# Kernel optimization log

Hardware: AMD Instinct MI355X
Metric: run time of the kernel (lower is better)

## Reference

```python
import jax, jax.numpy as jnp
import numpy as np

N, E, B = 24000, 96000, 1200
NPG = N // B  # nodes per graph

def _lin(k, fi, fo):
    s = 1.0 / np.sqrt(fi)
    return jax.random.uniform(k, (fi, fo), jnp.float32, -s, s)

def setup_inputs():
    key = jax.random.key(0)
    ks = jax.random.split(key, 32)
    x = jax.random.normal(ks[0], (N, 9), jnp.float32)
    edge_attr = jax.random.normal(ks[1], (E, 4), jnp.float32)
    src = jax.random.randint(ks[2], (E,), 0, N)
    # destination node within the same graph as the source (block-diagonal adjacency)
    dst = (src // NPG) * NPG + jax.random.randint(ks[3], (E,), 0, NPG)
    edge_index = jnp.stack([src, dst]).astype(jnp.int32)
    batch = (jnp.arange(N) // NPG).astype(jnp.int32)
    fp_batch = jax.random.normal(ks[4], (B, 2048), jnp.float32)
    p = dict(
        Wq1=_lin(ks[5], 9, 512), bq1=jnp.zeros(512, jnp.float32),
        Wk1=_lin(ks[6], 9, 512), bk1=jnp.zeros(512, jnp.float32),
        Wv1=_lin(ks[7], 9, 512), bv1=jnp.zeros(512, jnp.float32),
        We1=_lin(ks[8], 4, 512),
        Ws1=_lin(ks[9], 9, 512), bs1=jnp.zeros(512, jnp.float32),
        Wq2=_lin(ks[10], 512, 1024), bq2=jnp.zeros(1024, jnp.float32),
        Wk2=_lin(ks[11], 512, 1024), bk2=jnp.zeros(1024, jnp.float32),
        Wv2=_lin(ks[12], 512, 1024), bv2=jnp.zeros(1024, jnp.float32),
        We2=_lin(ks[13], 4, 1024),
        Ws2=_lin(ks[14], 512, 1024), bs2=jnp.zeros(1024, jnp.float32),
        Wfp=_lin(ks[15], 2048, 256), bfp=jnp.zeros(256, jnp.float32),
        Wfin=_lin(ks[16], 1280, 1024), bfin=jnp.zeros(1024, jnp.float32),
    )
    return dict(x=x, edge_index=edge_index, edge_attr=edge_attr, batch=batch, fp_batch=fp_batch, **p)

def _tconv(x, src, dst, ea, Wq, bq, Wk, bk, Wv, bv, We, Ws, bs, H, C):
    """PyG TransformerConv: concat=True, beta=False, root_weight=True."""
    n = x.shape[0]
    q = (x @ Wq + bq).reshape(n, H, C)
    k = (x @ Wk + bk).reshape(n, H, C)
    v = (x @ Wv + bv).reshape(n, H, C)
    e = (ea @ We).reshape(-1, H, C)            # lin_edge has no bias
    ke = k[src] + e                            # [E,H,C]
    alpha = jnp.einsum('ehc,ehc->eh', q[dst], ke) / jnp.sqrt(jnp.float32(C))
    # scatter-softmax over incoming edges of each target node
    amax = jax.ops.segment_max(alpha, dst, num_segments=n)
    amax = jnp.where(jnp.isfinite(amax), amax, 0.0)  # nodes with no in-edges
    ex = jnp.exp(alpha - amax[dst])
    den = jax.ops.segment_sum(ex, dst, num_segments=n)[dst] + 1e-16
    msg = (v[src] + e) * (ex / den)[:, :, None]
    out = jax.ops.segment_sum(msg, dst, num_segments=n).reshape(n, H * C)
    return out + x @ Ws + bs                   # root/skip connection

def reference(x, edge_index, edge_attr, batch, fp_batch, Wq1, bq1, Wk1, bk1, Wv1, bv1, We1, Ws1, bs1, Wq2, bq2, Wk2, bk2, Wv2, bv2, We2, Ws2, bs2, Wfp, bfp, Wfin, bfin):
    src, dst = edge_index[0], edge_index[1]
    h = jax.nn.relu(_tconv(x, src, dst, edge_attr, Wq1, bq1, Wk1, bk1, Wv1, bv1, We1, Ws1, bs1, 4, 128))
    h = _tconv(h, src, dst, edge_attr, Wq2, bq2, Wk2, bk2, Wv2, bv2, We2, Ws2, bs2, 4, 256)
    cnt = jax.ops.segment_sum(jnp.ones((h.shape[0],), h.dtype), batch, num_segments=B)
    g = jax.ops.segment_sum(h, batch, num_segments=B) / cnt[:, None]  # global_mean_pool
    fp = fp_batch @ Wfp + bfp
    return jnp.concatenate([g, fp], axis=-1) @ Wfin + bfin
```

## Files before the change

kernel.cpp:

```cpp
#include <hip/hip_runtime.h>
#include <cstdint>
#include <cstddef>

static constexpr int NN = 24000;
static constexpr int NE = 96000;
static constexpr int NB = 1200;
static constexpr int NPG = 20;
static constexpr int MPAD = 24064;

typedef __attribute__((ext_vector_type(8))) short bfv8;
typedef __attribute__((ext_vector_type(4))) float fv4;

__device__ __forceinline__ unsigned f2ord(float f){
  unsigned u = __float_as_uint(f);
  return (u & 0x80000000u) ? ~u : (u | 0x80000000u);
}
__device__ __forceinline__ float ord2f(unsigned u){
  return (u & 0x80000000u) ? __uint_as_float(u & 0x7FFFFFFFu)
                           : __uint_as_float(~u);
}
__device__ __forceinline__ unsigned short f2bf(float f){
  unsigned u = __float_as_uint(f);
  u += 0x7FFFu + ((u >> 16) & 1u);
  return (unsigned short)(u >> 16);
}
__device__ __forceinline__ float bf2f(unsigned short s){
  return __uint_as_float(((unsigned)s) << 16);
}

__global__ __launch_bounds__(256) void count_kernel(const int* __restrict__ dst,
                                                    unsigned* __restrict__ deg)
{
  int e = blockIdx.x*256 + threadIdx.x;
  if (e < NE) atomicAdd(&deg[dst[e]], 1u);
}

__global__ __launch_bounds__(1024) void scan_kernel(const unsigned* __restrict__ deg,
                                                    unsigned* __restrict__ rowstart)
{
  __shared__ unsigned s[1024];
  __shared__ unsigned carry_s;
  int tid = threadIdx.x;
  if (tid == 0) carry_s = 0;
  __syncthreads();
  for (int base = 0; base < NN; base += 1024){
    unsigned v = (base + tid < NN) ? deg[base + tid] : 0u;
    s[tid] = v;
    __syncthreads();
#pragma unroll
    for (int off = 1; off < 1024; off <<= 1){
      unsigned t = (tid >= off) ? s[tid - off] : 0u;
      __syncthreads();
      s[tid] += t;
      __syncthreads();
    }
    unsigned carry = carry_s;
    if (base + tid < NN) rowstart[base + tid] = carry + s[tid] - v;
    __syncthreads();
    if (tid == 0) carry_s = carry + s[1023];
    __syncthreads();
  }
  if (tid == 0) rowstart[NN] = carry_s;
}

__global__ __launch_bounds__(256) void scatter_kernel(const int* __restrict__ dst,
                                                      const unsigned* __restrict__ rowstart,
                                                      unsigned* __restrict__ cur,
                                                      int* __restrict__ eidx)
{
  int e = blockIdx.x*256 + threadIdx.x;
  if (e >= NE) return;
  int d = dst[e];
  unsigned p = rowstart[d] + atomicAdd(&cur[d], 1u);
  eidx[p] = e;
}

__global__ __launch_bounds__(256) void node_gemm_l1_pair(
    const float* __restrict__ x,
    const float* __restrict__ Wa, const float* __restrict__ ba,
    const float* __restrict__ Wb, const float* __restrict__ bb,
    float* __restrict__ outa, float* __restrict__ outb)
{
  int t = blockIdx.x*256 + threadIdx.x;
  if (t >= NN*512) return;
  int n = t >> 9, j = t & 511;
  float xr[9];
#pragma unroll
  for (int i=0;i<9;i++) xr[i] = x[n*9+i];
  float aa=ba[j], ab=bb[j];
#pragma unroll
  for (int i=0;i<9;i++){
    float xi = xr[i];
    aa += xi*Wa[i*512+j];
    ab += xi*Wb[i*512+j];
  }
  outa[t]=aa; outb[t]=ab;
}

__global__ __launch_bounds__(256) void alpha_f32_kernel(
    const float* __restrict__ q, const float* __restrict__ k,
    const float* __restrict__ ea, const float* __restrict__ We,
    const int* __restrict__ src, const int* __restrict__ dst,
    float* __restrict__ alpha, unsigned* __restrict__ amax)
{
  constexpr int C = 128, HC = 512;
  int wave = (blockIdx.x*256 + threadIdx.x) >> 6;
  int lane = threadIdx.x & 63;
  if (wave >= NE) return;
  int e = wave;
  int s = src[e], d = dst[e];
  float ea0=ea[e*4+0], ea1=ea[e*4+1], ea2=ea[e*4+2], ea3=ea[e*4+3];
  const float scale = 1.0f / sqrtf((float)C);
#pragma unroll
  for (int h=0;h<4;h++){
    float part = 0.f;
#pragma unroll
    for (int c0=0;c0<C;c0+=64){
      int f = h*C + c0 + lane;
      float ke = k[(size_t)s*HC + f]
               + ea0*We[0*HC+f] + ea1*We[1*HC+f] + ea2*We[2*HC+f] + ea3*We[3*HC+f];
      part += q[(size_t)d*HC + f] * ke;
    }
#pragma unroll
    for (int off=32; off>=1; off>>=1) part += __shfl_xor(part, off);
    if (lane==0){
      float a = part*scale;
      alpha[e*4+h] = a;
      atomicMax(&amax[d*4+h], f2ord(a));
    }
  }
}

__global__ __launch_bounds__(256) void alpha_bf16_kernel(
    const unsigned short* __restrict__ q, const unsigned short* __restrict__ k,
    const float* __restrict__ ea, const float* __restrict__ We,
    const int* __restrict__ src, const int* __restrict__ dst,
    float* __restrict__ alpha, unsigned* __restrict__ amax)
{
  int wave = (blockIdx.x*256 + threadIdx.x) >> 6;
  int lane = threadIdx.x & 63;
  if (wave >= NE) return;
  int e = wave;
  int s = src[e], d = dst[e];
  float ea0=ea[e*4+0], ea1=ea[e*4+1], ea2=ea[e*4+2], ea3=ea[e*4+3];
  const float scale = 1.0f/16.0f;
#pragma unroll
  for (int p=0;p<2;p++){
    int off = p*512 + lane*8;
    bfv8 qv = *reinterpret_cast<const bfv8*>(q + (size_t)d*1024 + off);
    bfv8 kv = *reinterpret_cast<const bfv8*>(k + (size_t)s*1024 + off);
    float part = 0.f;
#pragma unroll
    for (int j=0;j<8;j++){
      int f = off + j;
      float ef = ea0*We[f] + ea1*We[1024+f] + ea2*We[2048+f] + ea3*We[3072+f];
      part += bf2f((unsigned short)qv[j]) * (bf2f((unsigned short)kv[j]) + ef);
    }
#pragma unroll
    for (int o=16; o>=1; o>>=1) part += __shfl_xor(part, o);
    if ((lane & 31) == 0){
      int h = p*2 + (lane>>5);
      float a = part*scale;
      alpha[e*4+h] = a;
      atomicMax(&amax[d*4+h], f2ord(a));
    }
  }
}

__global__ __launch_bounds__(256) void ex_kernel(
    float* __restrict__ alpha, const unsigned* __restrict__ amax,
    const int* __restrict__ dst, float* __restrict__ den)
{
  int t = blockIdx.x*256 + threadIdx.x;
  if (t >= NE*4) return;
  int e = t>>2, h = t&3;
  int d = dst[e];
  float m = ord2f(amax[d*4+h]);
  float v = __expf(alpha[t]-m);
  alpha[t] = v;
  unsafeAtomicAdd(&den[d*4+h], v);
}

__global__ __launch_bounds__(256) void gather512_kernel(
    const float* __restrict__ v, const float* __restrict__ ea,
    const float* __restrict__ We,
    const int* __restrict__ src,
    const unsigned* __restrict__ rowstart, const int* __restrict__ eidx,
    const float* __restrict__ exw, const float* __restrict__ den,
    float* __restrict__ acc)
{
  int n = blockIdx.x;
  int tid = threadIdx.x;
  int h = tid >> 6;
  int f2 = tid*2;
  unsigned p0 = rowstart[n], p1 = rowstart[n+1];
  float2 W0 = *reinterpret_cast<const float2*>(We + 0*512 + f2);
  float2 W1 = *reinterpret_cast<const float2*>(We + 1*512 + f2);
  float2 W2 = *reinterpret_cast<const float2*>(We + 2*512 + f2);
  float2 W3 = *reinterpret_cast<const float2*>(We + 3*512 + f2);
  float rdn = 1.0f / (den[n*4+h] + 1e-16f);
  float2 s = *reinterpret_cast<float2*>(acc + (size_t)n*512 + f2);
  for (unsigned p = p0; p < p1; ++p){
    int e  = eidx[p];
    float w = exw[e*4+h] * rdn;
    float4 eav = *reinterpret_cast<const float4*>(ea + (size_t)e*4);
    float2 vv  = *reinterpret_cast<const float2*>(v + (size_t)src[e]*512 + f2);
    float efx = eav.x*W0.x + eav.y*W1.x + eav.z*W2.x + eav.w*W3.x;
    float efy = eav.x*W0.y + eav.y*W1.y + eav.z*W2.y + eav.w*W3.y;
    s.x += w*(vv.x + efx);
    s.y += w*(vv.y + efy);
  }
  *reinterpret_cast<float2*>(acc + (size_t)n*512 + f2) = s;
}

__global__ __launch_bounds__(256) void gather1024_kernel(
    const float* __restrict__ v, const float* __restrict__ ea,
    const float* __restrict__ We,
    const int* __restrict__ src,
    const unsigned* __restrict__ rowstart, const int* __restrict__ eidx,
    const float* __restrict__ exw, const float* __restrict__ den,
    float* __restrict__ acc)
{
  int n = blockIdx.x;
  int tid = threadIdx.x;
  int h = tid >> 6;
  int f4 = tid*4;
  unsigned p0 = rowstart[n], p1 = rowstart[n+1];
  float4 W0 = *reinterpret_cast<const float4*>(We + 0*1024 + f4);
  float4 W1 = *reinterpret_cast<const float4*>(We + 1*1024 + f4);
  float4 W2 = *reinterpret_cast<const float4*>(We + 2*1024 + f4);
  float4 W3 = *reinterpret_cast<const float4*>(We + 3*1024 + f4);
  float rdn = 1.0f / (den[n*4+h] + 1e-16f);
  float4 s = *reinterpret_cast<float4*>(acc + (size_t)n*1024 + f4);
  for (unsigned p = p0; p < p1; ++p){
    int e  = eidx[p];
    float w = exw[e*4+h] * rdn;
    float4 eav = *reinterpret_cast<const float4*>(ea + (size_t)e*4);
    float4 vv  = *reinterpret_cast<const float4*>(v + (size_t)src[e]*1024 + f4);
    s.x += w*(vv.x + eav.x*W0.x + eav.y*W1.x + eav.z*W2.x + eav.w*W3.x);
    s.y += w*(vv.y + eav.x*W0.y + eav.y*W1.y + eav.z*W2.y + eav.w*W3.y);
    s.z += w*(vv.z + eav.x*W0.z + eav.y*W1.z + eav.z*W2.z + eav.w*W3.z);
    s.w += w*(vv.w + eav.x*W0.w + eav.y*W1.w + eav.z*W2.w + eav.w*W3.w);
  }
  *reinterpret_cast<float4*>(acc + (size_t)n*1024 + f4) = s;
}

__global__ __launch_bounds__(256) void relu_kernel(float* __restrict__ a, size_t n)
{
  size_t t = (size_t)blockIdx.x*256 + threadIdx.x;
  if (t < n) a[t] = fmaxf(a[t], 0.0f);
}

__global__ __launch_bounds__(256) void cvt_bf16_kernel(const float* __restrict__ in,
                                                       unsigned short* __restrict__ out,
                                                       size_t n)
{
  size_t t = (size_t)blockIdx.x*256 + threadIdx.x;
  if (t < n) out[t] = f2bf(in[t]);
}

__global__ __launch_bounds__(256) void cvt_wt_kernel(const float* __restrict__ W,
                                                     unsigned short* __restrict__ Wt)
{
  int t = blockIdx.x*256 + threadIdx.x;
  if (t >= 1024*512) return;
  int n = t >> 9, k = t & 511;
  Wt[t] = f2bf(W[k*1024 + n]);
}

template<bool BOUT>
__global__ __launch_bounds__(256) void gemm_bf16_mfma(
    const unsigned short* __restrict__ A,
    const unsigned short* __restrict__ B,
    const float* __restrict__ bias,
    void* __restrict__ Cout, int M)
{
  constexpr int K = 512, N = 1024;
  __shared__ unsigned short As[128*32];
  __shared__ unsigned short Bs[128*32];
  int tid  = threadIdx.x;
  int wid  = tid >> 6, lane = tid & 63;
  int wr   = wid >> 1, wc = wid & 1;
  int bm   = blockIdx.y * 128, bn = blockIdx.x * 128;
  int l15  = lane & 15, kg = lane >> 4;

  int r0 = (wid*2+0)*16 + (lane>>2);
  int r1 = (wid*2+1)*16 + (lane>>2);
  int s0 = lane & 3;
  int kc0 = s0 ^ ((r0>>1)&3);
  int kc1 = s0 ^ ((r1>>1)&3);
  unsigned short* ldsA0 = As + (wid*2+0)*512;
  unsigned short* ldsA1 = As + (wid*2+1)*512;
  unsigned short* ldsB0 = Bs + (wid*2+0)*512;
  unsigned short* ldsB1 = Bs + (wid*2+1)*512;

  fv4 acc[4][4];
#pragma unroll
  for (int m=0;m<4;m++)
#pragma unroll
    for (int n=0;n<4;n++) acc[m][n] = (fv4){0.f,0.f,0.f,0.f};

  for (int k0 = 0; k0 < K; k0 += 32){
    __syncthreads();
    __builtin_amdgcn_global_load_lds(
        (const __attribute__((address_space(1))) void*)(A + (size_t)(bm+r0)*K + k0 + kc0*8),
        (__attribute__((address_space(3))) void*)ldsA0, 16, 0, 0);
    __builtin_amdgcn_global_load_lds(
        (const __attribute__((address_space(1))) void*)(A + (size_t)(bm+r1)*K + k0 + kc1*8),
        (__attribute__((address_space(3))) void*)ldsA1, 16, 0, 0);
    __builtin_amdgcn_global_load_lds(
        (const __attribute__((address_space(1))) void*)(B + (size_t)(bn+r0)*K + k0 + kc0*8),
        (__attribute__((address_space(3))) void*)ldsB0, 16, 0, 0);
    __builtin_amdgcn_global_load_lds(
        (const __attribute__((address_space(1))) void*)(B + (size_t)(bn+r1)*K + k0 + kc1*8),
        (__attribute__((address_space(3))) void*)ldsB1, 16, 0, 0);
    __syncthreads();
    bfv8 af[4], bfr[4];
#pragma unroll
    for (int m=0;m<4;m++){
      int r  = wr*64 + m*16 + l15;
      int sl = kg ^ ((r>>1)&3);
      af[m] = *reinterpret_cast<const bfv8*>(reinterpret_cast<char*>(As) + r*64 + sl*16);
    }
#pragma unroll
    for (int n=0;n<4;n++){
      int r  = wc*64 + n*16 + l15;
      int sl = kg ^ ((r>>1)&3);
      bfr[n] = *reinterpret_cast<const bfv8*>(reinterpret_cast<char*>(Bs) + r*64 + sl*16);
    }
#pragma unroll
    for (int m=0;m<4;m++)
#pragma unroll
      for (int n=0;n<4;n++)
        acc[m][n] = __builtin_amdgcn_mfma_f32_16x16x32_bf16(af[m], bfr[n], acc[m][n], 0, 0, 0);
  }
#pragma unroll
  for (int m=0;m<4;m++){
#pragma unroll
    for (int n=0;n<4;n++){
      int col = bn + wc*64 + n*16 + l15;
      float bcol = bias[col];
#pragma unroll
      for (int r=0;r<4;r++){
        int row = bm + wr*64 + m*16 + (lane>>4)*4 + r;
        if (row < M){
          float val = acc[m][n][r] + bcol;
          if (BOUT) ((unsigned short*)Cout)[(size_t)row*N + col] = f2bf(val);
          else      ((float*)Cout)[(size_t)row*N + col] = val;
        }
      }
    }
  }
}

__global__ __launch_bounds__(256) void sgemm_partial(
    const float* __restrict__ A, const float* __restrict__ W,
    float* __restrict__ P, int M, int N, int K, int kchunk, int zoff)
{
  __shared__ float As[32][68];
  __shared__ __align__(16) float Bs[32][64];
  int tid = threadIdx.x;
  int bm = blockIdx.y*64, bn = blockIdx.x*64;
  int kbeg = blockIdx.z*kchunk;
  int kend = min(kbeg + kchunk, K);
  float* Pz = P + (size_t)(zoff + blockIdx.z)*M*N;
  int ty = tid >> 4, tx = tid & 15;
  float acc[4][4] = {};
  for (int k0 = kbeg; k0 < kend; k0 += 32){
#pragma unroll
    for (int i=0;i<2;i++){
      int lin = tid + i*256;
      int r = lin >> 3;
      int kq = (lin & 7) * 4;
      float4 av = make_float4(0.f,0.f,0.f,0.f);
      int row = bm + r;
      if (row < M) av = *reinterpret_cast<const float4*>(A + (size_t)row*K + k0 + kq);
      As[kq+0][r]=av.x; As[kq+1][r]=av.y; As[kq+2][r]=av.z; As[kq+3][r]=av.w;
    }
#pragma unroll
    for (int i=0;i<2;i++){
      int lin = tid + i*256;
      int kr = lin >> 4;
      int c4 = (lin & 15) * 4;
      float4 wv = *reinterpret_cast<const float4*>(W + (size_t)(k0+kr)*N + bn + c4);
      *reinterpret_cast<float4*>(&Bs[kr][c4]) = wv;
    }
    __syncthreads();
#pragma unroll
    for (int kk=0;kk<32;kk++){
      float a[4], b[4];
#pragma unroll
      for (int i=0;i<4;i++) a[i] = As[kk][ty*4+i];
#pragma unroll
      for (int j=0;j<4;j++) b[j] = Bs[kk][tx*4+j];
#pragma unroll
      for (int i=0;i<4;i++)
#pragma unroll
        for (int j=0;j<4;j++) acc[i][j] += a[i]*b[j];
    }
    __syncthreads();
  }
#pragma unroll
  for (int i=0;i<4;i++){
    int row = bm + ty*4 + i;
    if (row >= M) break;
#pragma unroll
    for (int j=0;j<4;j++)
      Pz[(size_t)row*N + bn + tx*4 + j] = acc[i][j];
  }
}

__global__ __launch_bounds__(256) void reduce_add_kernel(
    const float* __restrict__ P, const float* __restrict__ bias,
    float* __restrict__ O, int total, int nz, int nmask)
{
  int t = blockIdx.x*256 + threadIdx.x;
  if (t >= total) return;
  float s = bias[t & nmask];
  for (int z = 0; z < nz; ++z) s += P[(size_t)z*total + t];
  O[t] = s;
}

__global__ __launch_bounds__(256) void pool_kernel(const float* __restrict__ h2,
                                                   float* __restrict__ g)
{
  int t = blockIdx.x*256 + threadIdx.x;
  if (t >= NB*256) return;
  int b = t >> 8, f4 = (t & 255) * 4;
  float4 s = make_float4(0.f,0.f,0.f,0.f);
#pragma unroll
  for (int i=0;i<NPG;i++){
    float4 v = *reinterpret_cast<const float4*>(h2 + (size_t)(b*NPG+i)*1024 + f4);
    s.x += v.x; s.y += v.y; s.z += v.z; s.w += v.w;
  }
  s.x *= (1.0f/NPG); s.y *= (1.0f/NPG); s.z *= (1.0f/NPG); s.w *= (1.0f/NPG);
  *reinterpret_cast<float4*>(g + (size_t)b*1024 + f4) = s;
}

extern "C" void kernel_launch(void* const* d_in, const int* in_sizes, int n_in,
                              void* d_out, int out_size, void* d_ws, size_t ws_size,
                              hipStream_t stream)
{
  const float* x    = (const float*)d_in[0];
  const int*   ei   = (const int*)d_in[1];
  const float* ea   = (const float*)d_in[2];
  const float* fpb  = (const float*)d_in[4];
  const float* Wq1  = (const float*)d_in[5];  const float* bq1 = (const float*)d_in[6];
  const float* Wk1  = (const float*)d_in[7];  const float* bk1 = (const float*)d_in[8];
  const float* Wv1  = (const float*)d_in[9];  const float* bv1 = (const float*)d_in[10];
  const float* We1  = (const float*)d_in[11];
  const float* Ws1  = (const float*)d_in[12]; const float* bs1 = (const float*)d_in[13];
  const float* Wq2  = (const float*)d_in[14]; const float* bq2 = (const float*)d_in[15];
  const float* Wk2  = (const float*)d_in[16]; const float* bk2 = (const float*)d_in[17];
  const float* Wv2  = (const float*)d_in[18]; const float* bv2 = (const float*)d_in[19];
  const float* We2  = (const float*)d_in[20];
  const float* Ws2  = (const float*)d_in[21]; const float* bs2 = (const float*)d_in[22];
  const float* Wfp  = (const float*)d_in[23]; const float* bfp = (const float*)d_in[24];
  const float* Wfin = (const float*)d_in[25]; const float* bfin= (const float*)d_in[26];
  const int* src = ei;
  const int* dst = ei + NE;
  float* out = (float*)d_out;

  const size_t F512  = (size_t)NN*512;
  const size_t F1024 = (size_t)NN*1024;
  float* base = (float*)d_ws;
  float* C_a = base;
  float* C_b = base + F1024;
  float* H   = base + 2*F1024;
  float* qv1 = C_a;
  unsigned short* q2b = (unsigned short*)C_a;
  unsigned short* k2b = (unsigned short*)C_b;
  unsigned short* hb  = (unsigned short*)H;
  unsigned short* WtQ = hb + (size_t)MPAD*512;
  unsigned short* WtK = WtQ + (size_t)1024*512;
  unsigned short* WtV = WtK + (size_t)1024*512;
  unsigned short* WtS = WtV + (size_t)1024*512;
  unsigned short* hbT = (unsigned short*)C_a;
  float* P1 = C_a;
  float* P2 = C_a + 5*(size_t)NB*1024;

  float* tail = base + 2*F1024 + F512;
  float*    alphab   = tail;
  unsigned* amax     = (unsigned*)(alphab + (size_t)NE*4);
  float*    den      = (float*)(amax + (size_t)NN*4);
  unsigned* deg      = (unsigned*)(den + (size_t)NN*4);
  unsigned* cur      = deg + NN;
  unsigned* rowstart = cur + NN;
  int*      eidx     = (int*)(rowstart + NN + 1);
  float*    g        = (float*)(eidx + NE);
  float*    fp       = g + (size_t)NB*1024;

  hipMemsetAsync(deg, 0, sizeof(unsigned)*NN, stream);
  hipMemsetAsync(cur, 0, sizeof(unsigned)*NN, stream);
  count_kernel<<<(NE+255)/256, 256, 0, stream>>>(dst, deg);
  scan_kernel<<<1, 1024, 0, stream>>>(deg, rowstart);
  scatter_kernel<<<(NE+255)/256, 256, 0, stream>>>(dst, rowstart, cur, eidx);

  hipMemsetAsync(amax, 0, sizeof(unsigned)*(size_t)NN*4, stream);
  hipMemsetAsync(den,  0, sizeof(float)*(size_t)NN*4, stream);

  node_gemm_l1_pair<<<(NN*512+255)/256, 256, 0, stream>>>(x, Wq1,bq1, Wk1,bk1, qv1, H);
  alpha_f32_kernel<<<NE/4, 256, 0, stream>>>(qv1, H, ea, We1, src, dst, alphab, amax);
  ex_kernel<<<(NE*4+255)/256, 256, 0, stream>>>(alphab, amax, dst, den);
  node_gemm_l1_pair<<<(NN*512+255)/256, 256, 0, stream>>>(x, Wv1,bv1, Ws1,bs1, qv1, H);
  gather512_kernel<<<NN, 256, 0, stream>>>(qv1, ea, We1, src, rowstart, eidx, alphab, den, H);
  relu_kernel<<<(int)((F512+255)/256), 256, 0, stream>>>(H, F512);

  cvt_bf16_kernel<<<(int)((F512+255)/256), 256, 0, stream>>>(H, hbT, F512);
  hipMemcpyAsync(hb, hbT, F512*sizeof(unsigned short), hipMemcpyDeviceToDevice, stream);
  hipMemsetAsync(hb + F512, 0, (size_t)(MPAD-NN)*512*sizeof(unsigned short), stream);
  cvt_wt_kernel<<<(1024*512+255)/256, 256, 0, stream>>>(Wq2, WtQ);
  cvt_wt_kernel<<<(1024*512+255)/256, 256, 0, stream>>>(Wk2, WtK);
  cvt_wt_kernel<<<(1024*512+255)/256, 256, 0, stream>>>(Wv2, WtV);
  cvt_wt_kernel<<<(1024*512+255)/256, 256, 0, stream>>>(Ws2, WtS);

  hipMemsetAsync(amax, 0, sizeof(unsigned)*(size_t)NN*4, stream);
  hipMemsetAsync(den,  0, sizeof(float)*(size_t)NN*4, stream);

  {
    dim3 grid(8, MPAD/128);
    gemm_bf16_mfma<true><<<grid, 256, 0, stream>>>(hb, WtQ, bq2, q2b, NN);
    gemm_bf16_mfma<true><<<grid, 256, 0, stream>>>(hb, WtK, bk2, k2b, NN);
  }
  alpha_bf16_kernel<<<NE/4, 256, 0, stream>>>(q2b, k2b, ea, We2, src, dst, alphab, amax);
  ex_kernel<<<(NE*4+255)/256, 256, 0, stream>>>(alphab, amax, dst, den);
  {
    dim3 grid(8, MPAD/128);
    gemm_bf16_mfma<false><<<grid, 256, 0, stream>>>(hb, WtV, bv2, C_a, NN);
    gemm_bf16_mfma<false><<<grid, 256, 0, stream>>>(hb, WtS, bs2, C_b, NN);
  }
  gather1024_kernel<<<NN, 256, 0, stream>>>(C_a, ea, We2, src, rowstart, eidx, alphab, den, C_b);

  pool_kernel<<<(NB*256+255)/256, 256, 0, stream>>>(C_b, g);

  {
    dim3 gfp(256/64, (NB+63)/64, 8);
    sgemm_partial<<<gfp, 256, 0, stream>>>(fpb, Wfp, P2, NB, 256, 2048, 256, 0);
    reduce_add_kernel<<<(NB*256+255)/256, 256, 0, stream>>>(P2, bfp, fp, NB*256, 8, 255);
  }
  {
    dim3 g1(1024/64, (NB+63)/64, 4);
    sgemm_partial<<<g1, 256, 0, stream>>>(g, Wfin, P1, NB, 1024, 1024, 256, 0);
    dim3 g2(1024/64, (NB+63)/64, 1);
    sgemm_partial<<<g2, 256, 0, stream>>>(fp, Wfin + (size_t)1024*1024, P1, NB, 1024, 256, 256, 4);
    reduce_add_kernel<<<(NB*1024+255)/256, 256, 0, stream>>>(P1, bfin, out, NB*1024, 5, 1023);
  }
}
```

Baseline: 922.7 us.

## Store layer-1 Q/K/V and layer-2 V in bf16, fuse relu+convert into gather

Layer-1 node projections for Q, K and V are written as bf16, and the layer-1 alpha kernel reads bf16 vectors with a 16-lane head reduction. The layer-1 gather now applies relu and writes bf16 output directly into the GEMM input buffer. This removes the separate relu, convert and memcpy kernels. The layer-2 V GEMM also emits bf16, so the gather reads half the bytes. The cost is lower precision in the attention logits and messages, plus reworked buffer aliasing.

```diff
diff --git a/kernel.cpp b/kernel.cpp
--- a/kernel.cpp
+++ b/kernel.cpp
@@ -75,11 +75,12 @@
   eidx[p] = e;
 }
 
+template<bool BA, bool BB>
 __global__ __launch_bounds__(256) void node_gemm_l1_pair(
     const float* __restrict__ x,
     const float* __restrict__ Wa, const float* __restrict__ ba,
     const float* __restrict__ Wb, const float* __restrict__ bb,
-    float* __restrict__ outa, float* __restrict__ outb)
+    void* __restrict__ outa, void* __restrict__ outb)
 {
   int t = blockIdx.x*256 + threadIdx.x;
   if (t >= NN*512) return;
@@ -94,44 +95,44 @@
     aa += xi*Wa[i*512+j];
     ab += xi*Wb[i*512+j];
   }
-  outa[t]=aa; outb[t]=ab;
-}
-
-__global__ __launch_bounds__(256) void alpha_f32_kernel(
-    const float* __restrict__ q, const float* __restrict__ k,
+  if (BA) ((unsigned short*)outa)[t] = f2bf(aa); else ((float*)outa)[t] = aa;
+  if (BB) ((unsigned short*)outb)[t] = f2bf(ab); else ((float*)outb)[t] = ab;
+}
+
+__global__ __launch_bounds__(256) void alpha_bf16_hc512(
+    const unsigned short* __restrict__ q, const unsigned short* __restrict__ k,
     const float* __restrict__ ea, const float* __restrict__ We,
     const int* __restrict__ src, const int* __restrict__ dst,
     float* __restrict__ alpha, unsigned* __restrict__ amax)
 {
-  constexpr int C = 128, HC = 512;
   int wave = (blockIdx.x*256 + threadIdx.x) >> 6;
   int lane = threadIdx.x & 63;
   if (wave >= NE) return;
   int e = wave;
   int s = src[e], d = dst[e];
   float ea0=ea[e*4+0], ea1=ea[e*4+1], ea2=ea[e*4+2], ea3=ea[e*4+3];
-  const float scale = 1.0f / sqrtf((float)C);
-#pragma unroll
-  for (int h=0;h<4;h++){
-    float part = 0.f;
-#pragma unroll
-    for (int c0=0;c0<C;c0+=64){
-      int f = h*C + c0 + lane;
-      float ke = k[(size_t)s*HC + f]
-               + ea0*We[0*HC+f] + ea1*We[1*HC+f] + ea2*We[2*HC+f] + ea3*We[3*HC+f];
-      part += q[(size_t)d*HC + f] * ke;
-    }
-#pragma unroll
-    for (int off=32; off>=1; off>>=1) part += __shfl_xor(part, off);
-    if (lane==0){
-      float a = part*scale;
-      alpha[e*4+h] = a;
-      atomicMax(&amax[d*4+h], f2ord(a));
-    }
-  }
-}
-
-__global__ __launch_bounds__(256) void alpha_bf16_kernel(
+  const float scale = 0.088388347648318447f;
+  int off = lane*8;
+  bfv8 qv = *reinterpret_cast<const bfv8*>(q + (size_t)d*512 + off);
+  bfv8 kv = *reinterpret_cast<const bfv8*>(k + (size_t)s*512 + off);
+  float part = 0.f;
+#pragma unroll
+  for (int j=0;j<8;j++){
+    int f = off + j;
+    float ef = ea0*We[f] + ea1*We[512+f] + ea2*We[1024+f] + ea3*We[1536+f];
+    part += bf2f((unsigned short)qv[j]) * (bf2f((unsigned short)kv[j]) + ef);
+  }
+#pragma unroll
+  for (int o=8; o>=1; o>>=1) part += __shfl_xor(part, o);
+  if ((lane & 15) == 0){
+    int h = lane >> 4;
+    float a = part*scale;
+    alpha[e*4+h] = a;
+    atomicMax(&amax[d*4+h], f2ord(a));
+  }
+}
+
+__global__ __launch_bounds__(256) void alpha_bf16_hc1024(
     const unsigned short* __restrict__ q, const unsigned short* __restrict__ k,
     const float* __restrict__ ea, const float* __restrict__ We,
     const int* __restrict__ src, const int* __restrict__ dst,
@@ -182,12 +183,12 @@
 }
 
 __global__ __launch_bounds__(256) void gather512_kernel(
-    const float* __restrict__ v, const float* __restrict__ ea,
+    const unsigned short* __restrict__ v, const float* __restrict__ ea,
     const float* __restrict__ We,
     const int* __restrict__ src,
     const unsigned* __restrict__ rowstart, const int* __restrict__ eidx,
     const float* __restrict__ exw, const float* __restrict__ den,
-    float* __restrict__ acc)
+    const float* __restrict__ accin, unsigned short* __restrict__ hb)
 {
   int n = blockIdx.x;
   int tid = threadIdx.x;
@@ -199,22 +200,25 @@
   float2 W2 = *reinterpret_cast<const float2*>(We + 2*512 + f2);
   float2 W3 = *reinterpret_cast<const float2*>(We + 3*512 + f2);
   float rdn = 1.0f / (den[n*4+h] + 1e-16f);
-  float2 s = *reinterpret_cast<float2*>(acc + (size_t)n*512 + f2);
+  float2 s = *reinterpret_cast<const float2*>(accin + (size_t)n*512 + f2);
   for (unsigned p = p0; p < p1; ++p){
     int e  = eidx[p];
     float w = exw[e*4+h] * rdn;
     float4 eav = *reinterpret_cast<const float4*>(ea + (size_t)e*4);
-    float2 vv  = *reinterpret_cast<const float2*>(v + (size_t)src[e]*512 + f2);
+    ushort2 vv = *reinterpret_cast<const ushort2*>(v + (size_t)src[e]*512 + f2);
     float efx = eav.x*W0.x + eav.y*W1.x + eav.z*W2.x + eav.w*W3.x;
     float efy = eav.x*W0.y + eav.y*W1.y + eav.z*W2.y + eav.w*W3.y;
-    s.x += w*(vv.x + efx);
-    s.y += w*(vv.y + efy);
-  }
-  *reinterpret_cast<float2*>(acc + (size_t)n*512 + f2) = s;
+    s.x += w*(bf2f(vv.x) + efx);
+    s.y += w*(bf2f(vv.y) + efy);
+  }
+  ushort2 o;
+  o.x = f2bf(fmaxf(s.x, 0.0f));
+  o.y = f2bf(fmaxf(s.y, 0.0f));
+  *reinterpret_cast<ushort2*>(hb + (size_t)n*512 + f2) = o;
 }
 
 __global__ __launch_bounds__(256) void gather1024_kernel(
-    const float* __restrict__ v, const float* __restrict__ ea,
+    const unsigned short* __restrict__ v, const float* __restrict__ ea,
     const float* __restrict__ We,
     const int* __restrict__ src,
     const unsigned* __restrict__ rowstart, const int* __restrict__ eidx,
@@ -236,27 +240,13 @@
     int e  = eidx[p];
     float w = exw[e*4+h] * rdn;
     float4 eav = *reinterpret_cast<const float4*>(ea + (size_t)e*4);
-    float4 vv  = *reinterpret_cast<const float4*>(v + (size_t)src[e]*1024 + f4);
-    s.x += w*(vv.x + eav.x*W0.x + eav.y*W1.x + eav.z*W2.x + eav.w*W3.x);
-    s.y += w*(vv.y + eav.x*W0.y + eav.y*W1.y + eav.z*W2.y + eav.w*W3.y);
-    s.z += w*(vv.z + eav.x*W0.z + eav.y*W1.z + eav.z*W2.z + eav.w*W3.z);
-    s.w += w*(vv.w + eav.x*W0.w + eav.y*W1.w + eav.z*W2.w + eav.w*W3.w);
+    ushort4 vv = *reinterpret_cast<const ushort4*>(v + (size_t)src[e]*1024 + f4);
+    s.x += w*(bf2f(vv.x) + eav.x*W0.x + eav.y*W1.x + eav.z*W2.x + eav.w*W3.x);
+    s.y += w*(bf2f(vv.y) + eav.x*W0.y + eav.y*W1.y + eav.z*W2.y + eav.w*W3.y);
+    s.z += w*(bf2f(vv.z) + eav.x*W0.z + eav.y*W1.z + eav.z*W2.z + eav.w*W3.z);
+    s.w += w*(bf2f(vv.w) + eav.x*W0.w + eav.y*W1.w + eav.z*W2.w + eav.w*W3.w);
   }
   *reinterpret_cast<float4*>(acc + (size_t)n*1024 + f4) = s;
-}
-
-__global__ __launch_bounds__(256) void relu_kernel(float* __restrict__ a, size_t n)
-{
-  size_t t = (size_t)blockIdx.x*256 + threadIdx.x;
-  if (t < n) a[t] = fmaxf(a[t], 0.0f);
-}
-
-__global__ __launch_bounds__(256) void cvt_bf16_kernel(const float* __restrict__ in,
-                                                       unsigned short* __restrict__ out,
-                                                       size_t n)
-{
-  size_t t = (size_t)blockIdx.x*256 + threadIdx.x;
-  if (t < n) out[t] = f2bf(in[t]);
 }
 
 __global__ __launch_bounds__(256) void cvt_wt_kernel(const float* __restrict__ W,
@@ -467,15 +457,19 @@
   float* C_a = base;
   float* C_b = base + F1024;
   float* H   = base + 2*F1024;
-  float* qv1 = C_a;
+  unsigned short* q1b = (unsigned short*)C_a;
+  unsigned short* v1b = (unsigned short*)C_a;
+  unsigned short* k1b = (unsigned short*)H;
+  float*          s1  = H;
+  unsigned short* hb  = (unsigned short*)C_a + F1024;
   unsigned short* q2b = (unsigned short*)C_a;
   unsigned short* k2b = (unsigned short*)C_b;
-  unsigned short* hb  = (unsigned short*)H;
-  unsigned short* WtQ = hb + (size_t)MPAD*512;
+  unsigned short* v2b = (unsigned short*)C_a;
+  float*          s2  = C_b;
+  unsigned short* WtQ = (unsigned short*)H;
   unsigned short* WtK = WtQ + (size_t)1024*512;
   unsigned short* WtV = WtK + (size_t)1024*512;
   unsigned short* WtS = WtV + (size_t)1024*512;
-  unsigned short* hbT = (unsigned short*)C_a;
   float* P1 = C_a;
   float* P2 = C_a + 5*(size_t)NB*1024;
 
@@ -499,16 +493,16 @@
   hipMemsetAsync(amax, 0, sizeof(unsigned)*(size_t)NN*4, stream);
   hipMemsetAsync(den,  0, sizeof(float)*(size_t)NN*4, stream);
 
-  node_gemm_l1_pair<<<(NN*512+255)/256, 256, 0, stream>>>(x, Wq1,bq1, Wk1,bk1, qv1, H);
-  alpha_f32_kernel<<<NE/4, 256, 0, stream>>>(qv1, H, ea, We1, src, dst, alphab, amax);
+  node_gemm_l1_pair<true,true><<<(NN*512+255)/256, 256, 0, stream>>>(
+      x, Wq1,bq1, Wk1,bk1, q1b, k1b);
+  alpha_bf16_hc512<<<NE/4, 256, 0, stream>>>(q1b, k1b, ea, We1, src, dst, alphab, amax);
   ex_kernel<<<(NE*4+255)/256, 256, 0, stream>>>(alphab, amax, dst, den);
-  node_gemm_l1_pair<<<(NN*512+255)/256, 256, 0, stream>>>(x, Wv1,bv1, Ws1,bs1, qv1, H);
-  gather512_kernel<<<NN, 256, 0, stream>>>(qv1, ea, We1, src, rowstart, eidx, alphab, den, H);
-  relu_kernel<<<(int)((F512+255)/256), 256, 0, stream>>>(H, F512);
-
-  cvt_bf16_kernel<<<(int)((F512+255)/256), 256, 0, stream>>>(H, hbT, F512);
-  hipMemcpyAsync(hb, hbT, F512*sizeof(unsigned short), hipMemcpyDeviceToDevice, stream);
+  node_gemm_l1_pair<true,false><<<(NN*512+255)/256, 256, 0, stream>>>(
+      x, Wv1,bv1, Ws1,bs1, v1b, s1);
+  gather512_kernel<<<NN, 256, 0, stream>>>(v1b, ea, We1, src, rowstart, eidx,
+                                           alphab, den, s1, hb);
   hipMemsetAsync(hb + F512, 0, (size_t)(MPAD-NN)*512*sizeof(unsigned short), stream);
+
   cvt_wt_kernel<<<(1024*512+255)/256, 256, 0, stream>>>(Wq2, WtQ);
   cvt_wt_kernel<<<(1024*512+255)/256, 256, 0, stream>>>(Wk2, WtK);
   cvt_wt_kernel<<<(1024*512+255)/256, 256, 0, stream>>>(Wv2, WtV);
@@ -522,16 +516,17 @@
     gemm_bf16_mfma<true><<<grid, 256, 0, stream>>>(hb, WtQ, bq2, q2b, NN);
     gemm_bf16_mfma<true><<<grid, 256, 0, stream>>>(hb, WtK, bk2, k2b, NN);
   }
-  alpha_bf16_kernel<<<NE/4, 256, 0, stream>>>(q2b, k2b, ea, We2, src, dst, alphab, amax);
+  alpha_bf16_hc1024<<<NE/4, 256, 0, stream>>>(q2b, k2b, ea, We2, src, dst, alphab, amax);
   ex_kernel<<<(NE*4+255)/256, 256, 0, stream>>>(alphab, amax, dst, den);
   {
     dim3 grid(8, MPAD/128);
-    gemm_bf16_mfma<false><<<grid, 256, 0, stream>>>(hb, WtV, bv2, C_a, NN);
-    gemm_bf16_mfma<false><<<grid, 256, 0, stream>>>(hb, WtS, bs2, C_b, NN);
-  }
-  gather1024_kernel<<<NN, 256, 0, stream>>>(C_a, ea, We2, src, rowstart, eidx, alphab, den, C_b);
-
-  pool_kernel<<<(NB*256+255)/256, 256, 0, stream>>>(C_b, g);
+    gemm_bf16_mfma<true><<<grid, 256, 0, stream>>>(hb, WtV, bv2, v2b, NN);
+    gemm_bf16_mfma<false><<<grid, 256, 0, stream>>>(hb, WtS, bs2, s2, NN);
+  }
+  gather1024_kernel<<<NN, 256, 0, stream>>>(v2b, ea, We2, src, rowstart, eidx,
+                                            alphab, den, s2);
+
+  pool_kernel<<<(NB*256+255)/256, 256, 0, stream>>>(s2, g);
 
   {
     dim3 gfp(256/64, (NB+63)/64, 8);
```

Measured after the change: 827.8 us. -10.3%, faster.
